# Kernel optimization log

Measured on AMD Instinct MI355X. Metric: run time of the kernel, lower is better.

The kernel has to match this reference:

```python
import jax, jax.numpy as jnp
import numpy as np

LEVELS = 9
NLPOW = 1.4
BORDER_INV = 0.9
MIN_SHAPE = 5
PATCH = 4
EPS = 1e-8


def shift2(x, dy, dx):
    # out[..., u, v] = x[..., u - dy, v - dx], zero padded
    H, W = x.shape[-2], x.shape[-1]
    pad = [(0, 0)] * (x.ndim - 2) + [(max(dy, 0), max(-dy, 0)), (max(dx, 0), max(-dx, 0))]
    xp = jnp.pad(x, pad)
    return xp[..., max(-dy, 0):max(-dy, 0) + H, max(-dx, 0):max(-dx, 0) + W]


def maxpool2(x):
    # F.max_pool2d(x, 3, padding=1, stride=2) over the last two (target-image) dims
    return jax.lax.reduce_window(x, jnp.array(-jnp.inf, x.dtype), jax.lax.max,
                                 (1, 1, 3, 3), (1, 1, 2, 2),
                                 [(0, 0), (0, 0), (1, 1), (1, 1)])


def activation(c):
    # corr.clamp_(min=0).pow_(nlpow)
    return jnp.maximum(c, 0.0) ** NLPOW


def first_level(desc1, desc2):
    C, H1, W1 = desc1.shape[1:]
    H2, W2 = desc2.shape[2:]
    p = PATCH
    # F.unfold(desc1, 4, stride=4): non-overlapping 4x4 patches, row-major over (H1//4, W1//4)
    patches = desc1[0].reshape(C, H1 // p, p, W1 // p, p).transpose(1, 3, 0, 2, 4)
    patches = patches.reshape(-1, C, p, p)                       # (N, C, 4, 4)
    # normalized cross-correlation of every patch with desc2, padding 2 -> (H2+1, W2+1)
    num = jax.lax.conv_general_dilated(desc2, patches, (1, 1), [(2, 2), (2, 2)])  # (1, N, H2+1, W2+1)
    pnorm = jnp.sqrt(jnp.sum(patches ** 2, axis=(1, 2, 3)))      # (N,) patch norms
    sq = jnp.sum(desc2 ** 2, axis=1, keepdims=True)              # (1, 1, H2, W2)
    ones = jnp.ones((1, 1, p, p), desc2.dtype)
    wnorm = jnp.sqrt(jax.lax.conv_general_dilated(sq, ones, (1, 1), [(2, 2), (2, 2)]))
    corr = num / (pnorm[None, :, None, None] * wnorm + EPS)
    corr = corr.reshape(H1 // p, W1 // p, H2 + 1, W2 + 1)
    weights = (pnorm > 0).astype(corr.dtype).reshape(H1 // p, W1 // p)
    return corr, weights


def sparse_conv_fwd(corr, weights):
    # DeepMatching-style 2x2 children aggregation with validity weights.
    # corr: (H1, W1, h, w); weights: (H1, W1). Parent grid is ceil-halved.
    H1, W1 = corr.shape[:2]
    Hp, Wp = -(-H1 // 2), -(-W1 // 2)
    corr = jnp.pad(corr, [(0, 2 * Hp - H1), (0, 2 * Wp - W1), (0, 0), (0, 0)])
    weights = jnp.pad(weights, [(0, 2 * Hp - H1), (0, 2 * Wp - W1)])
    num = 0.0
    den = 0.0
    for di in (0, 1):
        for dj in (0, 1):
            w = weights[di::2, dj::2]
            num = num + w[..., None, None] * shift2(corr[di::2, dj::2], 2 * di - 1, 2 * dj - 1)
            den = den + w
    # border_inv normalization: interior patches divide by 4, borders by >= 4*0.9
    out = num / jnp.maximum(den, 4.0 * BORDER_INV)[..., None, None]
    return out, den * 0.25


def sparse_conv_rev(upper):
    # reverse aggregation: scatter parent maps back to the 2x2 children with inverse shifts
    Hp, Wp, hp, wp = upper.shape
    out = jnp.zeros((2 * Hp, 2 * Wp, hp, wp), upper.dtype)
    for di in (0, 1):
        for dj in (0, 1):
            out = out.at[di::2, dj::2].set(shift2(upper, 1 - 2 * di, 1 - 2 * dj))
    return out


def max_unpool(up, lower):
    # route parent scores back to the argmax locations of the 3x3/stride-2 max-pool of `lower`
    mp = maxpool2(lower)                                  # (H1, W1, hp, wp)
    h, w = lower.shape[-2:]
    ui = jnp.minimum(jnp.arange(h) // 2, mp.shape[-2] - 1)
    vi = jnp.minimum(jnp.arange(w) // 2, mp.shape[-1] - 1)
    up_mp = mp[..., ui[:, None], vi[None, :]]             # pooled max broadcast to full res
    up_val = up[..., ui[:, None], vi[None, :]]            # parent value broadcast to full res
    return jnp.where(lower == up_mp, jnp.maximum(lower, up_val), lower)


def pump_forward(desc1, desc2):
    corr, weights = first_level(desc1, desc2)
    pyramid = [activation(corr)]
    for level in range(1, LEVELS + 1):
        pooled = maxpool2(pyramid[-1])
        upper, weights = sparse_conv_fwd(pooled, weights)
        pyramid.append(activation(upper))
        if min(upper.shape[-2:]) <= MIN_SHAPE:
            break
    for level in range(len(pyramid) - 1, 0, -1):
        lo = pyramid[level - 1]
        rev = sparse_conv_rev(pyramid[level])[:lo.shape[0], :lo.shape[1]]
        pyramid[level - 1] = max_unpool(rev, lo)
        pyramid.pop()
    return pyramid[0]


def setup_inputs():
    key = jax.random.key(0)
    k1, k2 = jax.random.split(key)
    C, H, W = 128, 128, 128
    desc1 = jax.random.normal(k1, (1, C, H, W), jnp.float32)
    desc2 = jax.random.normal(k2, (1, C, H, W), jnp.float32)
    # PUMP pixel descriptors are L2-normalized per pixel
    desc1 = desc1 / (jnp.linalg.norm(desc1, axis=1, keepdims=True) + 1e-8)
    desc2 = desc2 / (jnp.linalg.norm(desc2, axis=1, keepdims=True) + 1e-8)
    return {"desc1": desc1, "desc2": desc2}


def reference(desc1, desc2):
    # refined full-resolution 4D correlation volume (H1//4, W1//4, H2+1, W2+1)
    return pump_forward(desc1, desc2)
```

## Files before the change

### kernel.cpp

```cpp
#include <hip/hip_runtime.h>
#include <hip/hip_fp16.h>
#include <math.h>

typedef unsigned int uint;
typedef unsigned short ushort;
typedef short f16x8 __attribute__((ext_vector_type(8)));
typedef float f32x4 __attribute__((ext_vector_type(4)));

#define NLPOW 1.4f
#define EPSF 1e-8f
#define HO 129

__device__ __forceinline__ float activate(float c) {
    c = fmaxf(c, 0.0f);
    return powf(c, NLPOW);
}

__device__ __forceinline__ void f16split(float v, ushort& h, ushort& l) {
    __half hv = __float2half(v);
    h = __half_as_ushort(hv);
    float r = (v - __half2float(hv)) * 2048.0f;
    l = __half_as_ushort(__float2half(r));
}

__device__ __forceinline__ void gld_lds16(const ushort* g, ushort* l) {
    __builtin_amdgcn_global_load_lds(
        (const __attribute__((address_space(1))) void*)g,
        (__attribute__((address_space(3))) void*)l,
        16, 0, 0);
}

__global__ void prep_d2(const float* __restrict__ d2, ushort* __restrict__ d2p) {
    int idx = blockIdx.x * 256 + threadIdx.x;
    if (idx >= 140 * 148 * 128) return;
    int c = idx & 127;
    int xp = (idx >> 7) % 148;
    int yp = idx / (148 * 128);
    int y = yp - 2, x = xp - 2;
    float v = 0.f;
    if ((unsigned)y < 128u && (unsigned)x < 128u)
        v = d2[c * 16384 + y * 128 + x];
    ushort h, lo;
    f16split(v, h, lo);
    long o = ((long)(yp * 148 + xp)) * 256 + c;
    d2p[o] = h;
    d2p[o + 128] = lo;
}

__global__ void build_Afrag(const float* __restrict__ d1, ushort* __restrict__ Ag) {
    int idx = blockIdx.x * 256 + threadIdx.x;
    if (idx >= 8 * 64 * 2 * 128 * 40) return;
    int kk = idx % 40;
    int row = (idx / 40) % 128;
    int pl = (idx / 5120) % 2;
    int s = (idx / 10240) % 64;
    int mb = idx / 655360;
    ushort hv = 0, lv = 0;
    if (kk < 32) {
        int kp = s * 32 + kk;
        int c = kp & 127;
        int ab = kp >> 7;
        int a = ab >> 2, b = ab & 3;
        int p = mb * 128 + row;
        int i = p >> 5, j = p & 31;
        float v = d1[c * 16384 + (4 * i + a) * 128 + (4 * j + b)];
        f16split(v, hv, lv);
    }
    Ag[idx] = pl ? lv : hv;
}

__global__ void pnorm_k(const float* __restrict__ d1, float* __restrict__ pn) {
    int p = blockIdx.x;
    int t = threadIdx.x;
    int i = p >> 5, j = p & 31;
    int pix = t & 15;
    int a = pix >> 2, b = pix & 3;
    int cg = t >> 4;
    const float* base = d1 + (4 * i + a) * 128 + (4 * j + b);
    float s = 0.f;
    for (int c = cg * 32; c < cg * 32 + 32; ++c) {
        float v = base[c * 16384];
        s += v * v;
    }
    #pragma unroll
    for (int off = 32; off > 0; off >>= 1) s += __shfl_down(s, off);
    if (t == 0) pn[p] = sqrtf(s);
}

__global__ void sq_k(const float* __restrict__ d2, float* __restrict__ sq) {
    int idx = blockIdx.x * 256 + threadIdx.x;
    if (idx >= 16384) return;
    float s = 0.f;
    for (int c = 0; c < 128; ++c) {
        float v = d2[c * 16384 + idx];
        s += v * v;
    }
    sq[idx] = s;
}

__global__ void wnorm_k(const float* __restrict__ sq, float* __restrict__ wnorm) {
    int idx = blockIdx.x * 256 + threadIdx.x;
    if (idx >= HO * HO) return;
    int y = idx / HO, x = idx % HO;
    float s = 0.f;
    #pragma unroll
    for (int a = 0; a < 4; ++a) {
        int yy = y - 2 + a;
        if ((unsigned)yy >= 128u) continue;
        #pragma unroll
        for (int b = 0; b < 4; ++b) {
            int xx = x - 2 + b;
            if ((unsigned)xx >= 128u) continue;
            s += sq[yy * 128 + xx];
        }
    }
    wnorm[idx] = sqrtf(s);
}

__global__ __launch_bounds__(256, 2) void conv_mfma(
    const ushort* __restrict__ Ag,
    const ushort* __restrict__ d2p,
    const float* __restrict__ pn, const float* __restrict__ wnorm,
    float* __restrict__ out)
{
    __shared__ __align__(16) ushort A2[2][2][5120];
    __shared__ __align__(16) ushort B2[2][2][5120];

    const int t = threadIdx.x;
    const int mb = blockIdx.x & 7;
    const int nb = blockIdx.x >> 3;
    const int ny0 = (nb / 9) * 8;
    const int nx0 = (nb % 9) * 16;
    const int p0 = mb * 128;

    const int l = t & 63;
    const int w = t >> 6;
    const int wm = w & 1, wn_ = w >> 1;
    const int lm = l & 15, lg = l >> 4;

    const int bn = t >> 1;
    const int bh = t & 1;
    const int bdy = bn >> 4;
    const int bx = bn & 15;

    f32x4 accH[4][4] = {};
    f32x4 accX[4][4] = {};
    uint4 Wh0, Wh1, Wl0, Wl1;

    auto stageA = [&](int s, int cur) {
        const ushort* src = Ag + (long)(mb * 64 + s) * 10240;
        ushort* dst = &A2[cur][0][0];
        #pragma unroll
        for (int i = 0; i < 5; ++i)
            gld_lds16(src + (i * 256 + t) * 8, dst + (i * 256 + t) * 8);
    };
    auto loadB = [&](int s) {
        int ab = s >> 2;
        int a = ab >> 2, b = ab & 3, c0 = (s & 3) * 32;
        const ushort* src = d2p
            + ((long)(ny0 + bdy + a) * 148 + (nx0 + bx + b)) * 256 + c0 + bh * 16;
        Wh0 = *(const uint4*)src;
        Wh1 = *(const uint4*)(src + 8);
        Wl0 = *(const uint4*)(src + 128);
        Wl1 = *(const uint4*)(src + 136);
    };
    auto writeB = [&](int cur) {
        int ro = bn * 40 + bh * 16;
        ushort* dh = &B2[cur][0][0] + ro;
        ushort* dl = &B2[cur][1][0] + ro;
        *(uint4*)dh = Wh0;
        *(uint4*)(dh + 8) = Wh1;
        *(uint4*)dl = Wl0;
        *(uint4*)(dl + 8) = Wl1;
    };

    stageA(0, 0);
    loadB(0);
    writeB(0);
    __syncthreads();

    for (int s = 0; s < 64; ++s) {
        const int cur = s & 1;
        if (s < 63) { stageA(s + 1, cur ^ 1); loadB(s + 1); }

        f16x8 fah[4], fal[4];
        #pragma unroll
        for (int mi = 0; mi < 4; ++mi) {
            int ra = (wm * 64 + mi * 16 + lm) * 40 + lg * 8;
            fah[mi] = *(const f16x8*)(&A2[cur][0][0] + ra);
            fal[mi] = *(const f16x8*)(&A2[cur][1][0] + ra);
        }
        #pragma unroll
        for (int ni = 0; ni < 4; ++ni) {
            int rb = (wn_ * 64 + ni * 16 + lm) * 40 + lg * 8;
            f16x8 fbh = *(const f16x8*)(&B2[cur][0][0] + rb);
            f16x8 fbl = *(const f16x8*)(&B2[cur][1][0] + rb);
            #pragma unroll
            for (int mi = 0; mi < 4; ++mi) {
                accH[mi][ni] = __builtin_amdgcn_mfma_f32_16x16x32_f16(fah[mi], fbh, accH[mi][ni], 0, 0, 0);
                accX[mi][ni] = __builtin_amdgcn_mfma_f32_16x16x32_f16(fah[mi], fbl, accX[mi][ni], 0, 0, 0);
                accX[mi][ni] = __builtin_amdgcn_mfma_f32_16x16x32_f16(fal[mi], fbh, accX[mi][ni], 0, 0, 0);
            }
        }

        if (s < 63) writeB(cur ^ 1);
        __syncthreads();
    }

    #pragma unroll
    for (int mi = 0; mi < 4; ++mi) {
        #pragma unroll
        for (int ni = 0; ni < 4; ++ni) {
            int y = ny0 + wn_ * 4 + ni;
            int x = nx0 + lm;
            if (y < HO && x < HO) {
                float wv = wnorm[y * HO + x];
                f32x4 vh = accH[mi][ni];
                f32x4 vx = accX[mi][ni];
                #pragma unroll
                for (int r = 0; r < 4; ++r) {
                    int p = p0 + wm * 64 + mi * 16 + lg * 4 + r;
                    float num = vh[r] + vx[r] * (1.0f / 2048.0f);
                    float c = num / (pn[p] * wv + EPSF);
                    out[(long)p * (HO * HO) + y * HO + x] = activate(c);
                }
            }
        }
    }
}

__device__ __forceinline__ void maxpool_body(const float* __restrict__ in,
                                             float* __restrict__ out,
                                             int idx, int h, int hp) {
    int s = idx % hp;
    int r = (idx / hp) % hp;
    int g = idx / (hp * hp);
    const float* base = in + (long)g * h * h;
    int y0 = 2 * r - 1, x0 = 2 * s - 1;
    float m = -1e30f;
    #pragma unroll
    for (int dy = 0; dy < 3; ++dy) {
        int y = y0 + dy;
        if ((unsigned)y >= (unsigned)h) continue;
        #pragma unroll
        for (int dx = 0; dx < 3; ++dx) {
            int x = x0 + dx;
            if ((unsigned)x >= (unsigned)h) continue;
            m = fmaxf(m, base[y * h + x]);
        }
    }
    out[idx] = m;
}

__device__ __forceinline__ void sparse_body(const float* __restrict__ pooled,
                                            float* __restrict__ out,
                                            int idx, int G2, int h) {
    int x = idx % h;
    int y = (idx / h) % h;
    int J = (idx / (h * h)) % G2;
    int I = idx / (h * h * G2);
    int G = 2 * G2;
    float s = 0.f;
    #pragma unroll
    for (int di = 0; di < 2; ++di) {
        int yy = y + 1 - 2 * di;
        if ((unsigned)yy >= (unsigned)h) continue;
        #pragma unroll
        for (int dj = 0; dj < 2; ++dj) {
            int xx = x + 1 - 2 * dj;
            if ((unsigned)xx >= (unsigned)h) continue;
            s += pooled[((((2 * I + di) * G) + (2 * J + dj)) * (long)h + yy) * h + xx];
        }
    }
    out[idx] = activate(0.25f * s);
}

__device__ __forceinline__ void unpool_body(float* __restrict__ lo,
                                            const float* __restrict__ pooled,
                                            const float* __restrict__ up,
                                            int idx, int G, int hl, int hp) {
    int x = idx % hl;
    int y = (idx / hl) % hl;
    int gj = (idx / (hl * hl)) % G;
    int gi = idx / (hl * hl * G);
    float l = lo[idx];
    float m = pooled[(((long)gi * G + gj) * hp + (y >> 1)) * hp + (x >> 1)];
    if (l == m) {
        int ry = (y >> 1) - 1 + 2 * (gi & 1);
        int rx = (x >> 1) - 1 + 2 * (gj & 1);
        float uv = 0.f;
        if ((unsigned)ry < (unsigned)hp && (unsigned)rx < (unsigned)hp)
            uv = up[((((long)(gi >> 1)) * (G >> 1) + (gj >> 1)) * hp + ry) * hp + rx];
        lo[idx] = fmaxf(l, uv);
    }
}

__global__ void maxpool_k(const float* __restrict__ in, float* __restrict__ out,
                          int GG, int h, int hp) {
    int idx = blockIdx.x * 256 + threadIdx.x;
    if (idx >= GG * hp * hp) return;
    maxpool_body(in, out, idx, h, hp);
}

__global__ void sparse_fwd_k(const float* __restrict__ pooled, float* __restrict__ out,
                             int G2, int h) {
    int idx = blockIdx.x * 256 + threadIdx.x;
    if (idx >= G2 * G2 * h * h) return;
    sparse_body(pooled, out, idx, G2, h);
}

__global__ void unpool_k(float* __restrict__ lo, const float* __restrict__ pooled,
                         const float* __restrict__ up, int G, int hl, int hp) {
    int idx = blockIdx.x * 256 + threadIdx.x;
    if (idx >= G * G * hl * hl) return;
    unpool_body(lo, pooled, up, idx, G, hl, hp);
}

__global__ void small_levels(float* __restrict__ pyr2,
                             float* __restrict__ pool3, float* __restrict__ pyr3,
                             float* __restrict__ pool4, float* __restrict__ pyr4,
                             float* __restrict__ pool5, float* __restrict__ pyr5)
{
    const int t = threadIdx.x;
    for (int i = t; i < 64 * 17 * 17; i += 1024) maxpool_body(pyr2, pool3, i, 33, 17);
    __syncthreads();
    for (int i = t; i < 16 * 17 * 17; i += 1024) sparse_body(pool3, pyr3, i, 4, 17);
    __syncthreads();
    for (int i = t; i < 16 * 9 * 9; i += 1024) maxpool_body(pyr3, pool4, i, 17, 9);
    __syncthreads();
    for (int i = t; i < 4 * 9 * 9; i += 1024) sparse_body(pool4, pyr4, i, 2, 9);
    __syncthreads();
    for (int i = t; i < 4 * 5 * 5; i += 1024) maxpool_body(pyr4, pool5, i, 9, 5);
    __syncthreads();
    for (int i = t; i < 5 * 5; i += 1024) sparse_body(pool5, pyr5, i, 1, 5);
    __syncthreads();
    for (int i = t; i < 4 * 9 * 9; i += 1024) unpool_body(pyr4, pool5, pyr5, i, 2, 9, 5);
    __syncthreads();
    for (int i = t; i < 16 * 17 * 17; i += 1024) unpool_body(pyr3, pool4, pyr4, i, 4, 17, 9);
    __syncthreads();
    for (int i = t; i < 64 * 33 * 33; i += 1024) unpool_body(pyr2, pool3, pyr3, i, 8, 33, 17);
}

#define PN_OFF    0L
#define WN_OFF    1024L
#define SQ_OFF    17728L
#define CBASE     34112L
#define D2P_OFF   (CBASE)
#define AG_OFF    (CBASE + 2652160L)
#define POOL1_OFF (CBASE)
#define PYR1_OFF  (CBASE + 4326400L)
#define POOL2_OFF (CBASE + 5408000L)
#define PYR2_OFF  (CBASE + 5686784L)
#define POOL3_OFF (CBASE + 5756480L)
#define PYR3_OFF  (CBASE + 5774976L)
#define POOL4_OFF (CBASE + 5779600L)
#define PYR4_OFF  (CBASE + 5780896L)
#define POOL5_OFF (CBASE + 5781220L)
#define PYR5_OFF  (CBASE + 5781320L)

extern "C" void kernel_launch(void* const* d_in, const int* in_sizes, int n_in,
                              void* d_out, int out_size, void* d_ws, size_t ws_size,
                              hipStream_t stream) {
    const float* d1 = (const float*)d_in[0];
    const float* d2 = (const float*)d_in[1];
    float* out = (float*)d_out;
    float* ws = (float*)d_ws;

    float* pnf   = ws + PN_OFF;
    float* wnf   = ws + WN_OFF;
    float* sqf   = ws + SQ_OFF;
    ushort* d2p  = (ushort*)(ws + D2P_OFF);
    ushort* Ag   = (ushort*)(ws + AG_OFF);
    float* pool1 = ws + POOL1_OFF;
    float* pyr1  = ws + PYR1_OFF;
    float* pool2 = ws + POOL2_OFF;
    float* pyr2  = ws + PYR2_OFF;
    float* pool3 = ws + POOL3_OFF;
    float* pyr3  = ws + PYR3_OFF;
    float* pool4 = ws + POOL4_OFF;
    float* pyr4  = ws + PYR4_OFF;
    float* pool5 = ws + POOL5_OFF;
    float* pyr5  = ws + PYR5_OFF;

    prep_d2<<<(140 * 148 * 128 + 255) / 256, 256, 0, stream>>>(d2, d2p);
    build_Afrag<<<(8 * 64 * 2 * 128 * 40 + 255) / 256, 256, 0, stream>>>(d1, Ag);
    pnorm_k<<<1024, 64, 0, stream>>>(d1, pnf);
    sq_k<<<64, 256, 0, stream>>>(d2, sqf);
    wnorm_k<<<(HO * HO + 255) / 256, 256, 0, stream>>>(sqf, wnf);

    conv_mfma<<<8 * 153, 256, 0, stream>>>(Ag, d2p, pnf, wnf, out);

    maxpool_k<<<(1024 * 65 * 65 + 255) / 256, 256, 0, stream>>>(out, pool1, 1024, 129, 65);
    sparse_fwd_k<<<(256 * 65 * 65 + 255) / 256, 256, 0, stream>>>(pool1, pyr1, 16, 65);
    maxpool_k<<<(256 * 33 * 33 + 255) / 256, 256, 0, stream>>>(pyr1, pool2, 256, 65, 33);
    sparse_fwd_k<<<(64 * 33 * 33 + 255) / 256, 256, 0, stream>>>(pool2, pyr2, 8, 33);

    small_levels<<<1, 1024, 0, stream>>>(pyr2, pool3, pyr3, pool4, pyr4, pool5, pyr5);

    unpool_k<<<(256 * 4225 + 255) / 256, 256, 0, stream>>>(pyr1, pool2, pyr2, 16, 65, 33);
    unpool_k<<<(1024 * 16641 + 255) / 256, 256, 0, stream>>>(out, pool1, pyr1, 32, 129, 65);
}
```

Measured before the change: 586.1 us.

## Load B operand fragments directly from global into registers, drop B LDS staging

The B operand (shifted desc2 windows) is no longer staged through shared memory. Each lane now loads its MFMA fragments straight from global memory into a double-buffered register array. The main loop is unrolled by two so the A/B buffer index is a compile-time constant, and A addressing is precomputed. This removes the LDS writes and reads for B and halves LDS usage. In exchange it adds redundant global loads across waves (each wm pair loads the same B) and more register pressure from the extra uint4 buffers.

Result: slower. 691.1 us (+17.9%).

```diff
diff --git a/kernel.cpp b/kernel.cpp
--- a/kernel.cpp
+++ b/kernel.cpp
@@ -124,7 +124,6 @@
     float* __restrict__ out)
 {
     __shared__ __align__(16) ushort A2[2][2][5120];
-    __shared__ __align__(16) ushort B2[2][2][5120];
 
     const int t = threadIdx.x;
     const int mb = blockIdx.x & 7;
@@ -138,63 +137,48 @@
     const int wm = w & 1, wn_ = w >> 1;
     const int lm = l & 15, lg = l >> 4;
 
-    const int bn = t >> 1;
-    const int bh = t & 1;
-    const int bdy = bn >> 4;
-    const int bx = bn & 15;
-
     f32x4 accH[4][4] = {};
     f32x4 accX[4][4] = {};
-    uint4 Wh0, Wh1, Wl0, Wl1;
+
+    const ushort* aSrcT = Ag + (long)mb * 64 * 10240 + t * 8;
+    ushort* aDstT = &A2[0][0][0] + t * 8;
+    const ushort* aBase = &A2[0][0][0] + (wm * 64 + lm) * 40 + lg * 8;
+
+    const ushort* bNi[4];
+    #pragma unroll
+    for (int ni = 0; ni < 4; ++ni)
+        bNi[ni] = d2p + ((long)(ny0 + wn_ * 4 + ni) * 148 + (nx0 + lm)) * 256 + lg * 8;
+
+    uint4 B0[8], B1[8];
 
     auto stageA = [&](int s, int cur) {
-        const ushort* src = Ag + (long)(mb * 64 + s) * 10240;
-        ushort* dst = &A2[cur][0][0];
+        const ushort* src = aSrcT + (long)s * 10240;
+        ushort* dst = aDstT + cur * 10240;
         #pragma unroll
         for (int i = 0; i < 5; ++i)
-            gld_lds16(src + (i * 256 + t) * 8, dst + (i * 256 + t) * 8);
+            gld_lds16(src + i * 2048, dst + i * 2048);
     };
-    auto loadB = [&](int s) {
-        int ab = s >> 2;
-        int a = ab >> 2, b = ab & 3, c0 = (s & 3) * 32;
-        const ushort* src = d2p
-            + ((long)(ny0 + bdy + a) * 148 + (nx0 + bx + b)) * 256 + c0 + bh * 16;
-        Wh0 = *(const uint4*)src;
-        Wh1 = *(const uint4*)(src + 8);
-        Wl0 = *(const uint4*)(src + 128);
-        Wl1 = *(const uint4*)(src + 136);
+    auto loadB = [&](int s, uint4 (&B)[8]) {
+        const int ab = s >> 2;
+        const int uoff = ((ab >> 2) * 148 + (ab & 3)) * 256 + (s & 3) * 32;
+        #pragma unroll
+        for (int ni = 0; ni < 4; ++ni) {
+            const ushort* p = bNi[ni] + uoff;
+            B[ni * 2 + 0] = *(const uint4*)p;
+            B[ni * 2 + 1] = *(const uint4*)(p + 128);
+        }
     };
-    auto writeB = [&](int cur) {
-        int ro = bn * 40 + bh * 16;
-        ushort* dh = &B2[cur][0][0] + ro;
-        ushort* dl = &B2[cur][1][0] + ro;
-        *(uint4*)dh = Wh0;
-        *(uint4*)(dh + 8) = Wh1;
-        *(uint4*)dl = Wl0;
-        *(uint4*)(dl + 8) = Wl1;
-    };
-
-    stageA(0, 0);
-    loadB(0);
-    writeB(0);
-    __syncthreads();
-
-    for (int s = 0; s < 64; ++s) {
-        const int cur = s & 1;
-        if (s < 63) { stageA(s + 1, cur ^ 1); loadB(s + 1); }
-
+    auto mfmaStep = [&](int cur, const uint4 (&B)[8]) {
         f16x8 fah[4], fal[4];
         #pragma unroll
         for (int mi = 0; mi < 4; ++mi) {
-            int ra = (wm * 64 + mi * 16 + lm) * 40 + lg * 8;
-            fah[mi] = *(const f16x8*)(&A2[cur][0][0] + ra);
-            fal[mi] = *(const f16x8*)(&A2[cur][1][0] + ra);
+            fah[mi] = *(const f16x8*)(aBase + cur * 10240 + mi * 640);
+            fal[mi] = *(const f16x8*)(aBase + cur * 10240 + 5120 + mi * 640);
         }
         #pragma unroll
         for (int ni = 0; ni < 4; ++ni) {
-            int rb = (wn_ * 64 + ni * 16 + lm) * 40 + lg * 8;
-            f16x8 fbh = *(const f16x8*)(&B2[cur][0][0] + rb);
-            f16x8 fbl = *(const f16x8*)(&B2[cur][1][0] + rb);
+            f16x8 fbh = *(const f16x8*)&B[ni * 2 + 0];
+            f16x8 fbl = *(const f16x8*)&B[ni * 2 + 1];
             #pragma unroll
             for (int mi = 0; mi < 4; ++mi) {
                 accH[mi][ni] = __builtin_amdgcn_mfma_f32_16x16x32_f16(fah[mi], fbh, accH[mi][ni], 0, 0, 0);
@@ -202,8 +186,19 @@
                 accX[mi][ni] = __builtin_amdgcn_mfma_f32_16x16x32_f16(fal[mi], fbh, accX[mi][ni], 0, 0, 0);
             }
         }
-
-        if (s < 63) writeB(cur ^ 1);
+    };
+
+    stageA(0, 0);
+    loadB(0, B0);
+    __syncthreads();
+
+    for (int s = 0; s < 64; s += 2) {
+        if (s < 63) { stageA(s + 1, 1); loadB(s + 1, B1); }
+        mfmaStep(0, B0);
+        __syncthreads();
+
+        if (s < 62) { stageA(s + 2, 0); loadB(s + 2, B0); }
+        mfmaStep(1, B1);
         __syncthreads();
     }
 
```
